# Optimization experiments

Measured on AMD Instinct MI355X. Metric: run time of the kernel, lower is better.

The kernel has to match this reference:

```python
import jax, jax.numpy as jnp
import numpy as np

B = 512      # batch
L = 20       # reviews per user/item (L1 == L2)
N = 100      # words per review (must match between user/item, required by original bmm)
V = 50000    # vocab
D = 64       # word_dim
E = 32       # id_emb_size
U = 20000    # user_num
I = 20000    # item_num
H = 3        # point_num_heads
NT, NM = 10, 12  # travel type / month cardinalities


def _lin(x, W, b):
    # torch nn.Linear: x @ W.T + b, W is [out, in]
    return x @ W.T + b


def _hard_gumbel(logits, g):
    # F.gumbel_softmax(hard=True, tau=1, dim=1); g is pre-sampled standard Gumbel noise
    y = jax.nn.softmax(logits + g, axis=1)
    hard = jax.nn.one_hot(jnp.argmax(y, axis=1), logits.shape[1], dtype=y.dtype)
    return hard - jax.lax.stop_gradient(y) + y  # straight-through


def _coatt(u_fea, i_fea, M, Wu, bu, Wi, bi, pooling, gumbel_noise=None):
    # u_fea: [B, L1, d]; i_fea: [B, L2, d]
    u = _lin(u_fea, Wu, bu)
    i = _lin(i_fea, Wi, bi)
    S = jnp.einsum('bld,de,bme->blm', u, M, i)  # [B, L1, L2]
    if pooling == 'max':
        u_score, i_score = S.max(axis=2), S.max(axis=1)
    else:
        u_score, i_score = S.mean(axis=2), S.mean(axis=1)
    if gumbel_noise is not None:
        gu, gi = gumbel_noise
        p_u, p_i = _hard_gumbel(u_score, gu), _hard_gumbel(i_score, gi)
    else:
        p_u, p_i = jax.nn.softmax(u_score, axis=1), jax.nn.softmax(i_score, axis=1)
    return p_u[..., None], p_i[..., None]  # [B, L1, 1], [B, L2, 1]


def setup_inputs() -> dict:
    key = jax.random.key(0)
    ks = iter(jax.random.split(key, 48))
    unif = lambda shape, s=0.1: jax.random.uniform(next(ks), shape, minval=-s, maxval=s, dtype=jnp.float32)
    xav = lambda shape: jax.random.normal(next(ks), shape, dtype=jnp.float32) * np.sqrt(2.0 / (shape[-1] + shape[-2]))
    inp = {}
    inp['user_reviews'] = jax.random.randint(next(ks), (B, L, N), 0, V)
    inp['item_reviews'] = jax.random.randint(next(ks), (B, L, N), 0, V)
    inp['uids'] = jax.random.randint(next(ks), (B,), 0, U)
    inp['iids'] = jax.random.randint(next(ks), (B,), 0, I)
    inp['travel_type'] = jax.random.randint(next(ks), (B,), 0, NT)
    inp['travel_month'] = jax.random.randint(next(ks), (B,), 0, NM)
    # pre-sampled standard Gumbel noise for the hard pointer selection (one per head)
    inp['gnoise_u'] = -jnp.log(-jnp.log(jax.random.uniform(next(ks), (H, B, L), minval=1e-20, maxval=1.0)))
    inp['gnoise_i'] = -jnp.log(-jnp.log(jax.random.uniform(next(ks), (H, B, L), minval=1e-20, maxval=1.0)))
    # embedding tables
    inp['user_word_embs'] = unif((V, D))
    inp['item_word_embs'] = unif((V, D))
    inp['user_id_table'] = unif((U, E), 1.0)
    inp['item_id_table'] = unif((I, E), 1.0)
    inp['type_table'] = unif((NT, E), 1.0)
    inp['month_table'] = unif((NM, E), 1.0)
    # review gate
    inp['fc_g1_w'] = unif((D, D)); inp['fc_g1_b'] = unif((D,))
    inp['fc_g2_w'] = unif((D, D)); inp['fc_g2_b'] = unif((D,))
    # per-head co-attention params (stacked over H)
    inp['M_r'] = xav((H, D, D)); inp['Wu_r'] = unif((H, D, D)); inp['bu_r'] = unif((H, D))
    inp['Wi_r'] = unif((H, D, D)); inp['bi_r'] = unif((H, D))
    inp['M_w'] = xav((H, D, D)); inp['Wu_w'] = unif((H, D, D)); inp['bu_w'] = unif((H, D))
    inp['Wi_w'] = unif((H, D, D)); inp['bi_w'] = unif((H, D))
    inp['M_f'] = xav((H, E, E)); inp['Wu_f'] = unif((H, E, E)); inp['bu_f'] = unif((H, E))
    inp['Wi_f'] = unif((H, E, E)); inp['bi_f'] = unif((H, E))
    # projection layers
    inp['ufc_w'] = unif((E, D)); inp['ufc_b'] = unif((E,))
    inp['ifc_w'] = unif((E, D)); inp['ifc_b'] = unif((E,))
    inp['u_fc_w'] = unif((E, E * H)); inp['u_fc_b'] = unif((E,))
    inp['i_fc_w'] = unif((E, E * H)); inp['i_fc_b'] = unif((E,))
    return inp


def reference(user_reviews, item_reviews, uids, iids, travel_type, travel_month,
              gnoise_u, gnoise_i, user_word_embs, item_word_embs,
              user_id_table, item_id_table, type_table, month_table,
              fc_g1_w, fc_g1_b, fc_g2_w, fc_g2_b,
              M_r, Wu_r, bu_r, Wi_r, bi_r,
              M_w, Wu_w, bu_w, Wi_w, bi_w,
              M_f, Wu_f, bu_f, Wi_f, bi_f,
              ufc_w, ufc_b, ifc_w, ifc_b, u_fc_w, u_fc_b, i_fc_w, i_fc_b):
    # id-type embeddings -> feature stack [B, 4, E]
    user_id_emb = user_id_table[uids]
    item_id_emb = item_id_table[iids]
    type_emb = type_table[travel_type]
    month_emb = month_table[travel_month]
    feature_embedding = jnp.stack([user_id_emb, item_id_emb, type_emb, month_emb], axis=1)

    def review_gate(reviews_idx, table):
        s = table[reviews_idx].sum(axis=2)  # [B, L, N, D] -> [B, L, D]
        return jax.nn.sigmoid(_lin(s, fc_g1_w, fc_g1_b)) * jnp.tanh(_lin(s, fc_g2_w, fc_g2_b))

    u_reviews_g = review_gate(user_reviews, user_word_embs)
    i_reviews_g = review_gate(item_reviews, item_word_embs)

    u_feas, i_feas = [], []
    for h in range(H):
        # review-level pointer co-attention (hard gumbel, max pooling)
        p_u, p_i = _coatt(u_reviews_g, i_reviews_g, M_r[h], Wu_r[h], bu_r[h], Wi_r[h], bi_r[h],
                          pooling='max', gumbel_noise=(gnoise_u[h], gnoise_i[h]))
        # soft index -> cast to int (kills gradient, like torch .long()) -> word gather
        u_idx = jnp.einsum('bln,bl->bn', user_reviews.astype(p_u.dtype), p_u[..., 0]).astype(jnp.int32)
        i_idx = jnp.einsum('bln,bl->bn', item_reviews.astype(p_i.dtype), p_i[..., 0]).astype(jnp.int32)
        u_words = user_word_embs[u_idx]  # [B, N, D]
        i_words = item_word_embs[i_idx]
        # word-level co-attention (softmax, avg pooling)
        p_u2, p_i2 = _coatt(u_words, i_words, M_w[h], Wu_w[h], bu_w[h], Wi_w[h], bi_w[h], pooling='avg')
        u_w_fea = jnp.einsum('bnd,bn->bd', u_words, p_u2[..., 0])
        i_w_fea = jnp.einsum('bnd,bn->bd', u_words, p_i2[..., 0])  # NOTE: original uses u_words here (kept)
        ure = jax.nn.relu(_lin(u_w_fea, ufc_w, ufc_b))  # dropout = identity (eval)
        ire = jax.nn.relu(_lin(i_w_fea, ifc_w, ifc_b))
        review_embedding = jnp.stack([ure, ire], axis=1)  # [B, 2, E]
        review_att, fea_att = _coatt(review_embedding, feature_embedding,
                                     M_f[h], Wu_f[h], bu_f[h], Wi_f[h], bi_f[h], pooling='avg')
        fea_att_e = feature_embedding * fea_att  # [B, 4, E]
        user_id_e, item_id_e, type_e, month_e = (fea_att_e[:, 0], fea_att_e[:, 1],
                                                 fea_att_e[:, 2], fea_att_e[:, 3])
        rae = review_embedding * review_att
        user_fea_h = rae[:, 0]
        u_feas.append(user_fea_h)
        i_feas.append(user_fea_h)  # NOTE: original assigns item_fea from the user slice (kept)
    u_out = _lin(jnp.concatenate(u_feas, axis=1), u_fc_w, u_fc_b)
    i_out = _lin(jnp.concatenate(i_feas, axis=1), i_fc_w, i_fc_b)
    user_fea = jnp.stack([user_id_e, type_e, u_out], axis=1)   # [B, 3, E]
    item_fea = jnp.stack([item_id_e, month_e, i_out], axis=1)  # [B, 3, E]
    return user_fea, item_fea
```

## Files before the change

### kernel.cpp

```cpp
#include <hip/hip_runtime.h>
#include <math.h>

#define Bn 512
#define Ln 20
#define Nn 100
#define Dn 64
#define En 32
#define Hn 3

__global__ __launch_bounds__(256) void k0a_prep(
    const float* __restrict__ M_r, const float* __restrict__ Wu_r, const float* __restrict__ bu_r,
    const float* __restrict__ Wi_r,
    const float* __restrict__ M_w, const float* __restrict__ Wu_w, const float* __restrict__ bu_w,
    const float* __restrict__ Wi_w, const float* __restrict__ bi_w,
    const float* __restrict__ Wu_f, const float* __restrict__ Wi_f,
    const float* __restrict__ ufc, const float* __restrict__ ifc,
    const float* __restrict__ ufc2, const float* __restrict__ ifc2,
    float* __restrict__ WiT_r, float* __restrict__ WMr, float* __restrict__ bMr,
    float* __restrict__ P, float* __restrict__ Q, float* __restrict__ MB, float* __restrict__ MTB,
    float* __restrict__ WuT_f, float* __restrict__ WiT_f,
    float* __restrict__ ufcT, float* __restrict__ ifcT,
    float* __restrict__ u_fcT, float* __restrict__ i_fcT)
{
    int t = blockIdx.x * blockDim.x + threadIdx.x;
    int stride = gridDim.x * blockDim.x;
    for (int k = t; k < Hn*Dn*Dn; k += stride) {
        int h = k >> 12, r = k & 4095; int c = r >> 6, e = r & 63;
        const float* Wu = Wu_r + h*4096; const float* M = M_r + h*4096;
        float a = 0.f;
        for (int d = 0; d < Dn; ++d) a += Wu[d*Dn + c] * M[d*Dn + e];
        WMr[k] = a;
    }
    for (int k = t; k < Hn*Dn*Dn; k += stride) {
        int h = k >> 12, r = k & 4095; int d = r >> 6, bb = r & 63;
        const float* M = M_w + h*4096; const float* Wi = Wi_w + h*4096;
        float a = 0.f;
        for (int e = 0; e < Dn; ++e) a += M[d*Dn + e] * Wi[e*Dn + bb];
        P[k] = a;
    }
    for (int k = t; k < Hn*Dn*Dn; k += stride) {
        int h = k >> 12, r = k & 4095; int d = r >> 6, bb = r & 63;
        const float* M = M_w + h*4096; const float* Wu = Wu_w + h*4096;
        float a = 0.f;
        for (int e = 0; e < Dn; ++e) a += M[e*Dn + d] * Wu[e*Dn + bb];
        Q[k] = a;
    }
    for (int k = t; k < Hn*Dn*Dn; k += stride) {
        int h = k >> 12, r = k & 4095; int c = r >> 6, dp = r & 63;
        WiT_r[k] = Wi_r[h*4096 + dp*Dn + c];
    }
    for (int k = t; k < Hn*Dn; k += stride) {
        int h = k >> 6, e = k & 63;
        const float* M = M_r + h*4096;
        float a = 0.f;
        for (int d = 0; d < Dn; ++d) a += bu_r[h*Dn + d] * M[d*Dn + e];
        bMr[k] = a;
        const float* Mw_ = M_w + h*4096;
        float p = 0.f, q = 0.f;
        for (int d2 = 0; d2 < Dn; ++d2) {
            p += Mw_[e*Dn + d2] * bi_w[h*Dn + d2];
            q += Mw_[d2*Dn + e] * bu_w[h*Dn + d2];
        }
        MB[k] = p; MTB[k] = q;
    }
    for (int k = t; k < Hn*En*En; k += stride) {
        int h = k / (En*En); int rem = k - h*En*En;
        int a = rem >> 5, c = rem & 31;
        int src = h*En*En + c*En + a;
        WuT_f[k] = Wu_f[src]; WiT_f[k] = Wi_f[src];
    }
    for (int k = t; k < Dn*En; k += stride) {
        int d = k >> 5, e = k & 31;
        ufcT[k] = ufc[e*Dn + d]; ifcT[k] = ifc[e*Dn + d];
    }
    for (int k = t; k < 96*En; k += stride) {
        int kk = k >> 5, e = k & 31;
        u_fcT[k] = ufc2[e*96 + kk]; i_fcT[k] = ifc2[e*96 + kk];
    }
}

__global__ __launch_bounds__(256) void k0b_prep(
    const float* __restrict__ Wu_w, const float* __restrict__ Wi_w,
    const float* __restrict__ P, const float* __restrict__ Q,
    const float* __restrict__ MB, const float* __restrict__ MTB,
    float* __restrict__ GuT, float* __restrict__ GiT,
    float* __restrict__ gu_v, float* __restrict__ gi_v)
{
    int t = blockIdx.x * blockDim.x + threadIdx.x;
    int stride = gridDim.x * blockDim.x;
    for (int k = t; k < Hn*Dn*Dn; k += stride) {
        int h = k >> 12, r = k & 4095; int bb = r >> 6, a = r & 63;
        const float* Wu = Wu_w + h*4096; const float* Pp = P + h*4096;
        float s = 0.f;
        for (int d = 0; d < Dn; ++d) s += Wu[d*Dn + a] * Pp[d*Dn + bb];
        GuT[k] = s;
    }
    for (int k = t; k < Hn*Dn*Dn; k += stride) {
        int h = k >> 12, r = k & 4095; int bb = r >> 6, a = r & 63;
        const float* Wi = Wi_w + h*4096; const float* Qp = Q + h*4096;
        float s = 0.f;
        for (int d = 0; d < Dn; ++d) s += Wi[d*Dn + a] * Qp[d*Dn + bb];
        GiT[k] = s;
    }
    for (int k = t; k < Hn*Dn; k += stride) {
        int h = k >> 6, a = k & 63;
        const float* Wu = Wu_w + h*4096; const float* Wi = Wi_w + h*4096;
        float s1 = 0.f, s2 = 0.f;
        for (int d = 0; d < Dn; ++d) {
            s1 += Wu[d*Dn + a] * MB[h*Dn + d];
            s2 += Wi[d*Dn + a] * MTB[h*Dn + d];
        }
        gu_v[k] = s1; gi_v[k] = s2;
    }
}

__global__ __launch_bounds__(256) void k1a_gsum(
    const int* __restrict__ urev, const int* __restrict__ irev,
    const float* __restrict__ utab, const float* __restrict__ itab,
    float* __restrict__ sout)
{
    int tid = threadIdx.x;
    int ln = tid & 63;
    int wv = tid >> 6;
    int gw = blockIdx.x * 4 + wv;
    int side = (gw >= Bn*Ln);
    int r = gw - (side ? Bn*Ln : 0);
    const int* rev = side ? irev : urev;
    const float* tab = side ? itab : utab;
    int i0 = rev[r*Nn + ln];
    int i1 = (ln < Nn - 64) ? rev[r*Nn + 64 + ln] : 0;
    int r0 = ln >> 4;
    int q4 = (ln & 15) << 2;
    float4 buf[25];
    #pragma unroll
    for (int j = 0; j < 25; ++j) {
        int n = r0 + 4*j;
        int idx = (n < 64) ? __shfl(i0, n) : __shfl(i1, n - 64);
        buf[j] = *(const float4*)(tab + idx*Dn + q4);
    }
    float4 a = buf[0];
    #pragma unroll
    for (int j = 1; j < 25; ++j) { a.x += buf[j].x; a.y += buf[j].y; a.z += buf[j].z; a.w += buf[j].w; }
    a.x += __shfl_xor(a.x, 16); a.y += __shfl_xor(a.y, 16); a.z += __shfl_xor(a.z, 16); a.w += __shfl_xor(a.w, 16);
    a.x += __shfl_xor(a.x, 32); a.y += __shfl_xor(a.y, 32); a.z += __shfl_xor(a.z, 32); a.w += __shfl_xor(a.w, 32);
    if (ln < 16) *(float4*)(sout + gw*Dn + q4) = a;
}

__global__ __launch_bounds__(256) void k1b_gate(
    const float* __restrict__ sin,
    const float* __restrict__ W1, const float* __restrict__ b1v,
    const float* __restrict__ W2, const float* __restrict__ b2v,
    float* __restrict__ ugo, float* __restrict__ igo)
{
    __shared__ float w1s[Dn][Dn+1];
    __shared__ float w2s[Dn][Dn+1];
    int tid = threadIdx.x;
    for (int k = tid; k < Dn*Dn; k += 256) {
        int r = k >> 6, c = k & 63;
        w1s[r][c] = W1[k]; w2s[r][c] = W2[k];
    }
    __syncthreads();
    int ln = tid & 63;
    int wv = tid >> 6;
    float b1 = b1v[ln], b2 = b2v[ln];
    int nW = gridDim.x * 4;
    for (int gw = blockIdx.x * 4 + wv; gw < 2*Bn*Ln; gw += nW) {
        float sv = sin[gw*Dn + ln];
        float t1 = b1, t2 = b2;
        #pragma unroll 8
        for (int d = 0; d < Dn; ++d) {
            float sd = __shfl(sv, d);
            t1 += sd * w1s[ln][d];
            t2 += sd * w2s[ln][d];
        }
        float g = (1.f / (1.f + expf(-t1))) * tanhf(t2);
        int side = (gw >= Bn*Ln);
        int r = gw - (side ? Bn*Ln : 0);
        (side ? igo : ugo)[r*Dn + ln] = g;
    }
}

__global__ __launch_bounds__(256) void k2_coatt(
    const int* __restrict__ urev, const int* __restrict__ irev,
    const int* __restrict__ uids, const int* __restrict__ iids,
    const int* __restrict__ ttype, const int* __restrict__ tmonth,
    const float* __restrict__ gu_all, const float* __restrict__ gi_all,
    const float* __restrict__ utab, const float* __restrict__ itab,
    const float* __restrict__ uid_tab, const float* __restrict__ iid_tab,
    const float* __restrict__ type_tab, const float* __restrict__ month_tab,
    const float* __restrict__ ug_in, const float* __restrict__ ig_in,
    const float* __restrict__ WMr, const float* __restrict__ bMr,
    const float* __restrict__ WiT_r, const float* __restrict__ bi_r,
    const float* __restrict__ GuT, const float* __restrict__ GiT,
    const float* __restrict__ gu_v, const float* __restrict__ gi_v,
    const float* __restrict__ M_f, const float* __restrict__ bu_f, const float* __restrict__ bi_f,
    const float* __restrict__ WuT_f, const float* __restrict__ WiT_f,
    const float* __restrict__ ufcT, const float* __restrict__ ufc_bv,
    const float* __restrict__ ifcT, const float* __restrict__ ifc_bv,
    float* __restrict__ feas, float* __restrict__ outp)
{
    __shared__ __align__(16) float big[13000];
    __shared__ float S[Ln][Ln];
    __shared__ int   lstar[2];
    __shared__ float vecs[4][Dn];
    __shared__ float sc[2][Nn];
    __shared__ float uif[2][Dn];
    __shared__ float re[2][En], fe[4][En];
    __shared__ float u3[2][En], i3[4][En], A3[2][En];
    __shared__ float att[6];

    float* ug_sp = big;
    float* ig_sp = big + 1280;
    float* pu_sp = big + 2560;
    float* pi_sp = big + 5120;
    float* Ab_sp = big + 7680;
    float* iv_sp = big + 8980;
    float* uw    = big;
    float* iw    = big + 6500;

    int tid = threadIdx.x;
    int bh = blockIdx.x;
    int b = bh / Hn;
    int h = bh - b*Hn;
    int ln = tid & 63;
    int wv = tid >> 6;

    if (tid < 4*En) {
        int rrow = tid >> 5, e = tid & 31;
        float v;
        if (rrow == 0) v = uid_tab[uids[b]*En + e];
        else if (rrow == 1) v = iid_tab[iids[b]*En + e];
        else if (rrow == 2) v = type_tab[ttype[b]*En + e];
        else v = month_tab[tmonth[b]*En + e];
        fe[rrow][e] = v;
    }
    {
        const float4* su = (const float4*)(ug_in + b*Ln*Dn);
        const float4* si = (const float4*)(ig_in + b*Ln*Dn);
        float4* du = (float4*)ug_sp;
        float4* di = (float4*)ig_sp;
        for (int k = tid; k < (Ln*Dn)/4; k += 256) { du[k] = su[k]; di[k] = si[k]; }
    }
    __syncthreads();

    {
        int mat = wv & 1;
        int dh  = wv >> 1;
        const float* W = (mat ? (WiT_r + h*4096) : (WMr + h*4096)) + dh*32*Dn + ln;
        const float* X = (mat ? ig_sp : ug_sp) + dh*32;
        float acc[Ln];
        #pragma unroll
        for (int l = 0; l < Ln; ++l) acc[l] = 0.f;
        for (int dd = 0; dd < 32; dd += 4) {
            float w0 = W[(dd+0)*Dn];
            float w1 = W[(dd+1)*Dn];
            float w2 = W[(dd+2)*Dn];
            float w3 = W[(dd+3)*Dn];
            #pragma unroll
            for (int l = 0; l < Ln; ++l) {
                float4 x = *(const float4*)(X + l*Dn + dd);
                acc[l] += x.x*w0 + x.y*w1 + x.z*w2 + x.w*w3;
            }
        }
        float* po = (mat ? pi_sp : pu_sp) + dh*(Ln*Dn) + ln;
        #pragma unroll
        for (int l = 0; l < Ln; ++l) po[l*Dn] = acc[l];
    }
    __syncthreads();
    for (int k = tid; k < 2*Ln*Dn; k += 256) {
        int mm = (k >= Ln*Dn);
        int r = k - (mm ? Ln*Dn : 0);
        int l = r >> 6, ee = r & 63;
        if (!mm) Ab_sp[l*65 + ee] = pu_sp[l*Dn + ee] + pu_sp[Ln*Dn + l*Dn + ee] + bMr[h*Dn + ee];
        else     iv_sp[l*65 + ee] = pi_sp[l*Dn + ee] + pi_sp[Ln*Dn + l*Dn + ee] + bi_r[h*Dn + ee];
    }
    __syncthreads();
    for (int k = tid; k < Ln*Ln; k += 256) {
        int l = k / Ln, m = k - l*Ln;
        float a = 0.f;
        for (int e = 0; e < Dn; ++e) a += Ab_sp[l*65 + e] * iv_sp[m*65 + e];
        S[l][m] = a;
    }
    __syncthreads();
    if (wv == 0) {
        float v = -3.4e38f;
        if (ln < Ln) {
            float mx = S[ln][0];
            #pragma unroll
            for (int m = 1; m < Ln; ++m) mx = fmaxf(mx, S[ln][m]);
            v = mx + gu_all[(h*Bn + b)*Ln + ln];
        }
        int idx = ln;
        #pragma unroll
        for (int off = 32; off > 0; off >>= 1) {
            float ov = __shfl_down(v, off);
            int oi = __shfl_down(idx, off);
            if (ov > v || (ov == v && oi < idx)) { v = ov; idx = oi; }
        }
        if (ln == 0) lstar[0] = idx;
    } else if (wv == 1) {
        float v = -3.4e38f;
        if (ln < Ln) {
            float mx = S[0][ln];
            #pragma unroll
            for (int l = 1; l < Ln; ++l) mx = fmaxf(mx, S[l][ln]);
            v = mx + gi_all[(h*Bn + b)*Ln + ln];
        }
        int idx = ln;
        #pragma unroll
        for (int off = 32; off > 0; off >>= 1) {
            float ov = __shfl_down(v, off);
            int oi = __shfl_down(idx, off);
            if (ov > v || (ov == v && oi < idx)) { v = ov; idx = oi; }
        }
        if (ln == 0) lstar[1] = idx;
    }
    __syncthreads();
    {
        const int* up = urev + (b*Ln + lstar[0])*Nn;
        const int* ip = irev + (b*Ln + lstar[1])*Nn;
        for (int k = tid; k < (Nn*Dn)/4; k += 256) {
            int n = k >> 4, q = (k & 15) << 2;
            float4 vu = *(const float4*)(utab + up[n]*Dn + q);
            float4 vi = *(const float4*)(itab + ip[n]*Dn + q);
            float* du = uw + n*65 + q;
            du[0] = vu.x; du[1] = vu.y; du[2] = vu.z; du[3] = vu.w;
            float* di = iw + n*65 + q;
            di[0] = vi.x; di[1] = vi.y; di[2] = vi.z; di[3] = vi.w;
        }
    }
    __syncthreads();
    if (tid < Dn) {
        float a = 0.f;
        for (int n = 0; n < Nn; ++n) a += uw[n*65 + tid];
        vecs[0][tid] = a * (1.f/Nn);
    } else if (tid < 2*Dn) {
        int d = tid - Dn;
        float a = 0.f;
        for (int n = 0; n < Nn; ++n) a += iw[n*65 + d];
        vecs[1][d] = a * (1.f/Nn);
    }
    __syncthreads();
    if (tid < Dn) {
        float a = gu_v[h*Dn + tid];
        for (int bb = 0; bb < Dn; ++bb) a += GuT[h*4096 + bb*Dn + tid] * vecs[1][bb];
        vecs[2][tid] = a;
    } else if (tid < 2*Dn) {
        int aa = tid - Dn;
        float a = gi_v[h*Dn + aa];
        for (int bb = 0; bb < Dn; ++bb) a += GiT[h*4096 + bb*Dn + aa] * vecs[0][bb];
        vecs[3][aa] = a;
    }
    __syncthreads();
    if (tid < Nn) {
        float a = 0.f;
        for (int d = 0; d < Dn; ++d) a += uw[tid*65 + d] * vecs[2][d];
        sc[0][tid] = a;
    } else if (tid >= 128 && tid < 128 + Nn) {
        int n = tid - 128;
        float a = 0.f;
        for (int d = 0; d < Dn; ++d) a += iw[n*65 + d] * vecs[3][d];
        sc[1][n] = a;
    }
    __syncthreads();
    if (wv == 0 || wv == 2) {
        float* s = sc[wv >> 1];
        float x0 = s[ln];
        float x1 = (ln < Nn - 64) ? s[64 + ln] : -3.4e38f;
        float mx = fmaxf(x0, x1);
        #pragma unroll
        for (int off = 32; off > 0; off >>= 1) mx = fmaxf(mx, __shfl_xor(mx, off));
        float e0 = expf(x0 - mx);
        float e1 = (ln < Nn - 64) ? expf(x1 - mx) : 0.f;
        float sum = e0 + e1;
        #pragma unroll
        for (int off = 32; off > 0; off >>= 1) sum += __shfl_xor(sum, off);
        float inv = 1.f / sum;
        s[ln] = e0 * inv;
        if (ln < Nn - 64) s[64 + ln] = e1 * inv;
    }
    __syncthreads();
    if (tid < Dn) {
        float a = 0.f;
        for (int n = 0; n < Nn; ++n) a += sc[0][n] * uw[n*65 + tid];
        uif[0][tid] = a;
    } else if (tid < 2*Dn) {
        int d = tid - Dn;
        float a = 0.f;
        for (int n = 0; n < Nn; ++n) a += sc[1][n] * uw[n*65 + d];
        uif[1][d] = a;
    }
    __syncthreads();
    if (tid < En) {
        float a = ufc_bv[tid];
        for (int d = 0; d < Dn; ++d) a += uif[0][d] * ufcT[d*En + tid];
        re[0][tid] = fmaxf(a, 0.f);
    } else if (tid < 2*En) {
        int e = tid - En;
        float a = ifc_bv[e];
        for (int d = 0; d < Dn; ++d) a += uif[1][d] * ifcT[d*En + e];
        re[1][e] = fmaxf(a, 0.f);
    }
    __syncthreads();
    const float* WuTf = WuT_f + h*En*En;
    const float* WiTf = WiT_f + h*En*En;
    const float* Mf   = M_f  + h*En*En;
    const float* buf_ = bu_f + h*En;
    const float* bif_ = bi_f + h*En;
    if (tid < 2*En) {
        int l = tid >> 5, e = tid & 31;
        float a = buf_[e];
        for (int j = 0; j < En; ++j) a += re[l][j] * WuTf[j*En + e];
        u3[l][e] = a;
    } else if (tid < 6*En) {
        int t2 = tid - 2*En;
        int m = t2 >> 5, e = t2 & 31;
        float a = bif_[e];
        for (int j = 0; j < En; ++j) a += fe[m][j] * WiTf[j*En + e];
        i3[m][e] = a;
    }
    __syncthreads();
    if (tid < 2*En) {
        int l = tid >> 5, e = tid & 31;
        float a = 0.f;
        for (int d = 0; d < En; ++d) a += u3[l][d] * Mf[d*En + e];
        A3[l][e] = a;
    }
    __syncthreads();
    if (tid == 0) {
        float S3[2][4];
        for (int l = 0; l < 2; ++l)
            for (int m = 0; m < 4; ++m) {
                float a = 0.f;
                for (int e = 0; e < En; ++e) a += A3[l][e] * i3[m][e];
                S3[l][m] = a;
            }
        float us0 = (S3[0][0] + S3[0][1] + S3[0][2] + S3[0][3]) * 0.25f;
        float us1 = (S3[1][0] + S3[1][1] + S3[1][2] + S3[1][3]) * 0.25f;
        float mx = fmaxf(us0, us1);
        float e0 = expf(us0 - mx), e1 = expf(us1 - mx);
        float inv = 1.f / (e0 + e1);
        att[0] = e0 * inv; att[1] = e1 * inv;
        float is_[4]; float mxi = -3.4e38f;
        for (int m = 0; m < 4; ++m) { is_[m] = (S3[0][m] + S3[1][m]) * 0.5f; mxi = fmaxf(mxi, is_[m]); }
        float ssum = 0.f, ee[4];
        for (int m = 0; m < 4; ++m) { ee[m] = expf(is_[m] - mxi); ssum += ee[m]; }
        float invi = 1.f / ssum;
        for (int m = 0; m < 4; ++m) att[2 + m] = ee[m] * invi;
    }
    __syncthreads();
    if (tid < En) {
        feas[b*96 + h*En + tid] = re[0][tid] * att[0];
    }
    if (h == 2) {
        if (tid >= 32 && tid < 64)        { int e = tid - 32;  outp[b*96 + e]              = fe[0][e] * att[2]; }
        else if (tid >= 64 && tid < 96)   { int e = tid - 64;  outp[b*96 + 32 + e]         = fe[2][e] * att[4]; }
        else if (tid >= 96 && tid < 128)  { int e = tid - 96;  outp[Bn*96 + b*96 + e]      = fe[1][e] * att[3]; }
        else if (tid >= 128 && tid < 160) { int e = tid - 128; outp[Bn*96 + b*96 + 32 + e] = fe[3][e] * att[5]; }
    }
}

__global__ __launch_bounds__(64) void k3_final(
    const float* __restrict__ feas,
    const float* __restrict__ u_fcT, const float* __restrict__ u_fc_bv,
    const float* __restrict__ i_fcT, const float* __restrict__ i_fc_bv,
    float* __restrict__ outp)
{
    __shared__ float f[96];
    int b = blockIdx.x, tid = threadIdx.x;
    for (int k = tid; k < 96; k += 64) f[k] = feas[b*96 + k];
    __syncthreads();
    if (tid < 32) {
        float a = u_fc_bv[tid];
        for (int k = 0; k < 96; ++k) a += f[k] * u_fcT[k*32 + tid];
        outp[b*96 + 64 + tid] = a;
    } else {
        int e = tid - 32;
        float a = i_fc_bv[e];
        for (int k = 0; k < 96; ++k) a += f[k] * i_fcT[k*32 + e];
        outp[Bn*96 + b*96 + 64 + e] = a;
    }
}

extern "C" void kernel_launch(void* const* d_in, const int* in_sizes, int n_in,
                              void* d_out, int out_size, void* d_ws, size_t ws_size,
                              hipStream_t stream)
{
    const int* urev = (const int*)d_in[0];
    const int* irev = (const int*)d_in[1];
    const int* uids = (const int*)d_in[2];
    const int* iids = (const int*)d_in[3];
    const int* ttype = (const int*)d_in[4];
    const int* tmonth = (const int*)d_in[5];
    const float* gu = (const float*)d_in[6];
    const float* gi = (const float*)d_in[7];
    const float* utab = (const float*)d_in[8];
    const float* itab = (const float*)d_in[9];
    const float* uid_tab = (const float*)d_in[10];
    const float* iid_tab = (const float*)d_in[11];
    const float* type_tab = (const float*)d_in[12];
    const float* month_tab = (const float*)d_in[13];
    const float* fc_g1_w = (const float*)d_in[14];
    const float* fc_g1_b = (const float*)d_in[15];
    const float* fc_g2_w = (const float*)d_in[16];
    const float* fc_g2_b = (const float*)d_in[17];
    const float* M_r = (const float*)d_in[18];
    const float* Wu_r = (const float*)d_in[19];
    const float* bu_r = (const float*)d_in[20];
    const float* Wi_r = (const float*)d_in[21];
    const float* bi_r = (const float*)d_in[22];
    const float* M_w = (const float*)d_in[23];
    const float* Wu_w = (const float*)d_in[24];
    const float* bu_w = (const float*)d_in[25];
    const float* Wi_w = (const float*)d_in[26];
    const float* bi_w = (const float*)d_in[27];
    const float* M_f = (const float*)d_in[28];
    const float* Wu_f = (const float*)d_in[29];
    const float* bu_f = (const float*)d_in[30];
    const float* Wi_f = (const float*)d_in[31];
    const float* bi_f = (const float*)d_in[32];
    const float* ufc_w = (const float*)d_in[33];
    const float* ufc_b = (const float*)d_in[34];
    const float* ifc_w = (const float*)d_in[35];
    const float* ifc_b = (const float*)d_in[36];
    const float* u_fc_w = (const float*)d_in[37];
    const float* u_fc_b = (const float*)d_in[38];
    const float* i_fc_w = (const float*)d_in[39];
    const float* i_fc_b = (const float*)d_in[40];
    (void)in_sizes; (void)n_in; (void)out_size; (void)ws_size;

    float* ws = (float*)d_ws;
    float* ugo   = ws;
    float* igo   = ugo + Bn*Ln*Dn;
    float* sgat  = igo + Bn*Ln*Dn;
    float* feas  = sgat + 2*Bn*Ln*Dn;
    float* WiT_r = feas + Bn*96;
    float* WMr   = WiT_r + Hn*Dn*Dn;
    float* bMr   = WMr + Hn*Dn*Dn;
    float* P     = bMr + Hn*Dn;
    float* Q     = P + Hn*Dn*Dn;
    float* MB    = Q + Hn*Dn*Dn;
    float* MTB   = MB + Hn*Dn;
    float* GuT   = MTB + Hn*Dn;
    float* GiT   = GuT + Hn*Dn*Dn;
    float* gu_v  = GiT + Hn*Dn*Dn;
    float* gi_v  = gu_v + Hn*Dn;
    float* WuT_f = gi_v + Hn*Dn;
    float* WiT_f = WuT_f + Hn*En*En;
    float* ufcT  = WiT_f + Hn*En*En;
    float* ifcT  = ufcT + Dn*En;
    float* u_fcT = ifcT + Dn*En;
    float* i_fcT = u_fcT + 96*En;

    hipLaunchKernelGGL(k0a_prep, dim3(48), dim3(256), 0, stream,
        M_r, Wu_r, bu_r, Wi_r, M_w, Wu_w, bu_w, Wi_w, bi_w,
        Wu_f, Wi_f, ufc_w, ifc_w, u_fc_w, i_fc_w,
        WiT_r, WMr, bMr, P, Q, MB, MTB, WuT_f, WiT_f, ufcT, ifcT, u_fcT, i_fcT);

    hipLaunchKernelGGL(k0b_prep, dim3(48), dim3(256), 0, stream,
        Wu_w, Wi_w, P, Q, MB, MTB, GuT, GiT, gu_v, gi_v);

    hipLaunchKernelGGL(k1a_gsum, dim3(2*Bn*Ln/4), dim3(256), 0, stream,
        urev, irev, utab, itab, sgat);

    hipLaunchKernelGGL(k1b_gate, dim3(512), dim3(256), 0, stream,
        sgat, fc_g1_w, fc_g1_b, fc_g2_w, fc_g2_b, ugo, igo);

    hipLaunchKernelGGL(k2_coatt, dim3(Bn*Hn), dim3(256), 0, stream,
        urev, irev, uids, iids, ttype, tmonth, gu, gi, utab, itab,
        uid_tab, iid_tab, type_tab, month_tab, ugo, igo,
        WMr, bMr, WiT_r, bi_r, GuT, GiT, gu_v, gi_v,
        M_f, bu_f, bi_f, WuT_f, WiT_f,
        ufcT, ufc_b, ifcT, ifc_b, feas, (float*)d_out);

    hipLaunchKernelGGL(k3_final, dim3(Bn), dim3(64), 0, stream,
        feas, u_fcT, u_fc_b, i_fcT, i_fc_b, (float*)d_out);
}
```

Before: 326.5 us.

## Shrink coattention kernel shared memory and restructure word gathers for occupancy

Shrinks k2_coatt's shared memory from a roughly 52KB region to a 25KB pool. It does this by swapping padded arrays for XOR-swizzled layouts and splitting the review projection across waves by row rather than by reduction half, which removes the partial-sum reduction pass. Only the user review's words are staged in shared memory. The item review's words are gathered straight from global memory into registers and reduced with wave shuffles, and the second gather is repeated for the score step. The aim is to fit more blocks per CU (launch bounds set to 4) and drop a sync and reduction stage, at the cost of repeating global gathers for the item table.

Result: no change. 326.7 us (+0.1%).

```diff
diff --git a/kernel.cpp b/kernel.cpp
--- a/kernel.cpp
+++ b/kernel.cpp
@@ -180,7 +180,7 @@
     }
 }
 
-__global__ __launch_bounds__(256) void k2_coatt(
+__global__ __launch_bounds__(256, 4) void k2_coatt(
     const int* __restrict__ urev, const int* __restrict__ irev,
     const int* __restrict__ uids, const int* __restrict__ iids,
     const int* __restrict__ ttype, const int* __restrict__ tmonth,
@@ -199,24 +199,12 @@
     const float* __restrict__ ifcT, const float* __restrict__ ifc_bv,
     float* __restrict__ feas, float* __restrict__ outp)
 {
-    __shared__ __align__(16) float big[13000];
-    __shared__ float S[Ln][Ln];
-    __shared__ int   lstar[2];
+    __shared__ __align__(16) float pool[6400];
     __shared__ float vecs[4][Dn];
     __shared__ float sc[2][Nn];
     __shared__ float uif[2][Dn];
-    __shared__ float re[2][En], fe[4][En];
-    __shared__ float u3[2][En], i3[4][En], A3[2][En];
     __shared__ float att[6];
-
-    float* ug_sp = big;
-    float* ig_sp = big + 1280;
-    float* pu_sp = big + 2560;
-    float* pi_sp = big + 5120;
-    float* Ab_sp = big + 7680;
-    float* iv_sp = big + 8980;
-    float* uw    = big;
-    float* iw    = big + 6500;
+    __shared__ int   lstar[2];
 
     int tid = threadIdx.x;
     int bh = blockIdx.x;
@@ -225,69 +213,58 @@
     int ln = tid & 63;
     int wv = tid >> 6;
 
-    if (tid < 4*En) {
-        int rrow = tid >> 5, e = tid & 31;
-        float v;
-        if (rrow == 0) v = uid_tab[uids[b]*En + e];
-        else if (rrow == 1) v = iid_tab[iids[b]*En + e];
-        else if (rrow == 2) v = type_tab[ttype[b]*En + e];
-        else v = month_tab[tmonth[b]*En + e];
-        fe[rrow][e] = v;
-    }
     {
         const float4* su = (const float4*)(ug_in + b*Ln*Dn);
         const float4* si = (const float4*)(ig_in + b*Ln*Dn);
-        float4* du = (float4*)ug_sp;
-        float4* di = (float4*)ig_sp;
+        float4* du = (float4*)pool;
+        float4* di = (float4*)(pool + 1280);
         for (int k = tid; k < (Ln*Dn)/4; k += 256) { du[k] = su[k]; di[k] = si[k]; }
     }
     __syncthreads();
 
     {
-        int mat = wv & 1;
-        int dh  = wv >> 1;
-        const float* W = (mat ? (WiT_r + h*4096) : (WMr + h*4096)) + dh*32*Dn + ln;
-        const float* X = (mat ? ig_sp : ug_sp) + dh*32;
-        float acc[Ln];
-        #pragma unroll
-        for (int l = 0; l < Ln; ++l) acc[l] = 0.f;
-        for (int dd = 0; dd < 32; dd += 4) {
+        int iside = wv >> 1;
+        int lbase = (wv & 1) * 10;
+        const float* W = (iside ? (WiT_r + h*4096) : (WMr + h*4096)) + ln;
+        const float* X = pool + (iside ? 1280 : 0);
+        float bias = iside ? bi_r[h*Dn + ln] : bMr[h*Dn + ln];
+        float acc[10];
+        #pragma unroll
+        for (int l = 0; l < 10; ++l) acc[l] = 0.f;
+        for (int dd = 0; dd < Dn; dd += 4) {
             float w0 = W[(dd+0)*Dn];
             float w1 = W[(dd+1)*Dn];
             float w2 = W[(dd+2)*Dn];
             float w3 = W[(dd+3)*Dn];
             #pragma unroll
-            for (int l = 0; l < Ln; ++l) {
-                float4 x = *(const float4*)(X + l*Dn + dd);
+            for (int l = 0; l < 10; ++l) {
+                float4 x = *(const float4*)(X + (lbase+l)*Dn + dd);
                 acc[l] += x.x*w0 + x.y*w1 + x.z*w2 + x.w*w3;
             }
         }
-        float* po = (mat ? pi_sp : pu_sp) + dh*(Ln*Dn) + ln;
-        #pragma unroll
-        for (int l = 0; l < Ln; ++l) po[l*Dn] = acc[l];
-    }
-    __syncthreads();
-    for (int k = tid; k < 2*Ln*Dn; k += 256) {
-        int mm = (k >= Ln*Dn);
-        int r = k - (mm ? Ln*Dn : 0);
-        int l = r >> 6, ee = r & 63;
-        if (!mm) Ab_sp[l*65 + ee] = pu_sp[l*Dn + ee] + pu_sp[Ln*Dn + l*Dn + ee] + bMr[h*Dn + ee];
-        else     iv_sp[l*65 + ee] = pi_sp[l*Dn + ee] + pi_sp[Ln*Dn + l*Dn + ee] + bi_r[h*Dn + ee];
+        float* out = pool + (iside ? 3840 : 2560);
+        #pragma unroll
+        for (int l = 0; l < 10; ++l) {
+            int lg = lbase + l;
+            out[lg*Dn + (ln ^ lg)] = acc[l] + bias;
+        }
     }
     __syncthreads();
     for (int k = tid; k < Ln*Ln; k += 256) {
         int l = k / Ln, m = k - l*Ln;
-        float a = 0.f;
-        for (int e = 0; e < Dn; ++e) a += Ab_sp[l*65 + e] * iv_sp[m*65 + e];
-        S[l][m] = a;
+        const float* Ab = pool + 2560 + l*Dn;
+        const float* iv = pool + 3840 + m*Dn;
+        float a = 0.f;
+        for (int e = 0; e < Dn; ++e) a += Ab[e ^ l] * iv[e ^ m];
+        pool[5120 + k] = a;
     }
     __syncthreads();
     if (wv == 0) {
         float v = -3.4e38f;
         if (ln < Ln) {
-            float mx = S[ln][0];
+            float mx = pool[5120 + ln*Ln];
             #pragma unroll
-            for (int m = 1; m < Ln; ++m) mx = fmaxf(mx, S[ln][m]);
+            for (int m = 1; m < Ln; ++m) mx = fmaxf(mx, pool[5120 + ln*Ln + m]);
             v = mx + gu_all[(h*Bn + b)*Ln + ln];
         }
         int idx = ln;
@@ -301,9 +278,9 @@
     } else if (wv == 1) {
         float v = -3.4e38f;
         if (ln < Ln) {
-            float mx = S[0][ln];
+            float mx = pool[5120 + ln];
             #pragma unroll
-            for (int l = 1; l < Ln; ++l) mx = fmaxf(mx, S[l][ln]);
+            for (int l = 1; l < Ln; ++l) mx = fmaxf(mx, pool[5120 + l*Ln + ln]);
             v = mx + gi_all[(h*Bn + b)*Ln + ln];
         }
         int idx = ln;
@@ -316,31 +293,48 @@
         if (ln == 0) lstar[1] = idx;
     }
     __syncthreads();
-    {
-        const int* up = urev + (b*Ln + lstar[0])*Nn;
-        const int* ip = irev + (b*Ln + lstar[1])*Nn;
-        for (int k = tid; k < (Nn*Dn)/4; k += 256) {
-            int n = k >> 4, q = (k & 15) << 2;
-            float4 vu = *(const float4*)(utab + up[n]*Dn + q);
-            float4 vi = *(const float4*)(itab + ip[n]*Dn + q);
-            float* du = uw + n*65 + q;
-            du[0] = vu.x; du[1] = vu.y; du[2] = vu.z; du[3] = vu.w;
-            float* di = iw + n*65 + q;
-            di[0] = vi.x; di[1] = vi.y; di[2] = vi.z; di[3] = vi.w;
-        }
-    }
-    __syncthreads();
-    if (tid < Dn) {
-        float a = 0.f;
-        for (int n = 0; n < Nn; ++n) a += uw[n*65 + tid];
-        vecs[0][tid] = a * (1.f/Nn);
-    } else if (tid < 2*Dn) {
-        int d = tid - Dn;
-        float a = 0.f;
-        for (int n = 0; n < Nn; ++n) a += iw[n*65 + d];
-        vecs[1][d] = a * (1.f/Nn);
-    }
-    __syncthreads();
+
+    int rubase = (b*Ln + lstar[0])*Nn;
+    int ribase = (b*Ln + lstar[1])*Nn;
+    int r0 = ln >> 4;
+    int q4 = (ln & 15) << 2;
+    int idxr[25];
+
+    if (wv < 2) {
+        for (int k = tid; k < Nn*16; k += 128) {
+            int n = k >> 4, qi = k & 15;
+            int idx = urev[rubase + n];
+            float4 v = *(const float4*)(utab + idx*Dn + (qi << 2));
+            *(float4*)(pool + n*Dn + (((qi ^ (n & 15)) << 2))) = v;
+        }
+    } else {
+        const int* rev = (wv == 2) ? irev : urev;
+        const float* tab = (wv == 2) ? itab : utab;
+        int rb = (wv == 2) ? ribase : rubase;
+        #pragma unroll
+        for (int j = 0; j < 25; ++j) idxr[j] = rev[rb + r0 + 4*j];
+        float4 s = make_float4(0.f, 0.f, 0.f, 0.f);
+        #pragma unroll 5
+        for (int g = 0; g < 5; ++g) {
+            float4 v0 = *(const float4*)(tab + idxr[g*5+0]*Dn + q4);
+            float4 v1 = *(const float4*)(tab + idxr[g*5+1]*Dn + q4);
+            float4 v2 = *(const float4*)(tab + idxr[g*5+2]*Dn + q4);
+            float4 v3 = *(const float4*)(tab + idxr[g*5+3]*Dn + q4);
+            float4 v4 = *(const float4*)(tab + idxr[g*5+4]*Dn + q4);
+            s.x += v0.x+v1.x+v2.x+v3.x+v4.x;
+            s.y += v0.y+v1.y+v2.y+v3.y+v4.y;
+            s.z += v0.z+v1.z+v2.z+v3.z+v4.z;
+            s.w += v0.w+v1.w+v2.w+v3.w+v4.w;
+        }
+        s.x += __shfl_xor(s.x, 16); s.y += __shfl_xor(s.y, 16); s.z += __shfl_xor(s.z, 16); s.w += __shfl_xor(s.w, 16);
+        s.x += __shfl_xor(s.x, 32); s.y += __shfl_xor(s.y, 32); s.z += __shfl_xor(s.z, 32); s.w += __shfl_xor(s.w, 32);
+        if (ln < 16) {
+            float4 m = make_float4(s.x*(1.f/Nn), s.y*(1.f/Nn), s.z*(1.f/Nn), s.w*(1.f/Nn));
+            *(float4*)(&vecs[(wv == 2) ? 1 : 0][q4]) = m;
+        }
+    }
+    __syncthreads();
+
     if (tid < Dn) {
         float a = gu_v[h*Dn + tid];
         for (int bb = 0; bb < Dn; ++bb) a += GuT[h*4096 + bb*Dn + tid] * vecs[1][bb];
@@ -352,15 +346,49 @@
         vecs[3][aa] = a;
     }
     __syncthreads();
+
     if (tid < Nn) {
         float a = 0.f;
-        for (int d = 0; d < Dn; ++d) a += uw[tid*65 + d] * vecs[2][d];
+        const float* row = pool + tid*Dn;
+        int sw = tid & 15;
+        #pragma unroll
+        for (int qi = 0; qi < 16; ++qi) {
+            float4 w = *(const float4*)(&vecs[2][qi << 2]);
+            float4 x = *(const float4*)(row + ((qi ^ sw) << 2));
+            a += x.x*w.x + x.y*w.y + x.z*w.z + x.w*w.w;
+        }
         sc[0][tid] = a;
-    } else if (tid >= 128 && tid < 128 + Nn) {
-        int n = tid - 128;
-        float a = 0.f;
-        for (int d = 0; d < Dn; ++d) a += iw[n*65 + d] * vecs[3][d];
-        sc[1][n] = a;
+    } else if (wv == 2) {
+        float4 wq = *(const float4*)(&vecs[3][q4]);
+        #pragma unroll 5
+        for (int g = 0; g < 5; ++g) {
+            float p0, p1, p2, p3, p4;
+            {
+                float4 v0 = *(const float4*)(itab + idxr[g*5+0]*Dn + q4);
+                float4 v1 = *(const float4*)(itab + idxr[g*5+1]*Dn + q4);
+                float4 v2 = *(const float4*)(itab + idxr[g*5+2]*Dn + q4);
+                float4 v3 = *(const float4*)(itab + idxr[g*5+3]*Dn + q4);
+                float4 v4 = *(const float4*)(itab + idxr[g*5+4]*Dn + q4);
+                p0 = v0.x*wq.x + v0.y*wq.y + v0.z*wq.z + v0.w*wq.w;
+                p1 = v1.x*wq.x + v1.y*wq.y + v1.z*wq.z + v1.w*wq.w;
+                p2 = v2.x*wq.x + v2.y*wq.y + v2.z*wq.z + v2.w*wq.w;
+                p3 = v3.x*wq.x + v3.y*wq.y + v3.z*wq.z + v3.w*wq.w;
+                p4 = v4.x*wq.x + v4.y*wq.y + v4.z*wq.z + v4.w*wq.w;
+            }
+            #pragma unroll
+            for (int off = 1; off < 16; off <<= 1) {
+                p0 += __shfl_xor(p0, off); p1 += __shfl_xor(p1, off);
+                p2 += __shfl_xor(p2, off); p3 += __shfl_xor(p3, off);
+                p4 += __shfl_xor(p4, off);
+            }
+            if ((ln & 15) == 0) {
+                sc[1][r0 + 4*(g*5+0)] = p0;
+                sc[1][r0 + 4*(g*5+1)] = p1;
+                sc[1][r0 + 4*(g*5+2)] = p2;
+                sc[1][r0 + 4*(g*5+3)] = p3;
+                sc[1][r0 + 4*(g*5+4)] = p4;
+            }
+        }
     }
     __syncthreads();
     if (wv == 0 || wv == 2) {
@@ -380,51 +408,63 @@
         if (ln < Nn - 64) s[64 + ln] = e1 * inv;
     }
     __syncthreads();
-    if (tid < Dn) {
-        float a = 0.f;
-        for (int n = 0; n < Nn; ++n) a += sc[0][n] * uw[n*65 + tid];
-        uif[0][tid] = a;
-    } else if (tid < 2*Dn) {
-        int d = tid - Dn;
-        float a = 0.f;
-        for (int n = 0; n < Nn; ++n) a += sc[1][n] * uw[n*65 + d];
-        uif[1][d] = a;
-    }
-    __syncthreads();
+    if (tid < 2*Dn) {
+        int which = tid >> 6;
+        int d = tid & 63;
+        int qt = (d >> 2), dl = d & 3;
+        const float* p = sc[which];
+        float a = 0.f;
+        for (int n = 0; n < Nn; ++n)
+            a += p[n] * pool[n*Dn + ((qt ^ (n & 15)) << 2) + dl];
+        uif[which][d] = a;
+    }
+    __syncthreads();
+    float* fe_ = pool;
+    float* re_ = pool + 128;
+    float* u3_ = pool + 192;
+    float* i3_ = pool + 256;
+    float* A3_ = pool + 384;
     if (tid < En) {
         float a = ufc_bv[tid];
         for (int d = 0; d < Dn; ++d) a += uif[0][d] * ufcT[d*En + tid];
-        re[0][tid] = fmaxf(a, 0.f);
+        re_[tid] = fmaxf(a, 0.f);
     } else if (tid < 2*En) {
         int e = tid - En;
         float a = ifc_bv[e];
         for (int d = 0; d < Dn; ++d) a += uif[1][d] * ifcT[d*En + e];
-        re[1][e] = fmaxf(a, 0.f);
+        re_[En + e] = fmaxf(a, 0.f);
+    } else if (tid < 2*En + 4*En) {
+        int j = tid - 2*En;
+        int rrow = j >> 5, e = j & 31;
+        float v;
+        if (rrow == 0) v = uid_tab[uids[b]*En + e];
+        else if (rrow == 1) v = iid_tab[iids[b]*En + e];
+        else if (rrow == 2) v = type_tab[ttype[b]*En + e];
+        else v = month_tab[tmonth[b]*En + e];
+        fe_[j] = v;
     }
     __syncthreads();
     const float* WuTf = WuT_f + h*En*En;
     const float* WiTf = WiT_f + h*En*En;
     const float* Mf   = M_f  + h*En*En;
-    const float* buf_ = bu_f + h*En;
-    const float* bif_ = bi_f + h*En;
     if (tid < 2*En) {
         int l = tid >> 5, e = tid & 31;
-        float a = buf_[e];
-        for (int j = 0; j < En; ++j) a += re[l][j] * WuTf[j*En + e];
-        u3[l][e] = a;
+        float a = bu_f[h*En + e];
+        for (int j = 0; j < En; ++j) a += re_[l*En + j] * WuTf[j*En + e];
+        u3_[tid] = a;
     } else if (tid < 6*En) {
         int t2 = tid - 2*En;
         int m = t2 >> 5, e = t2 & 31;
-        float a = bif_[e];
-        for (int j = 0; j < En; ++j) a += fe[m][j] * WiTf[j*En + e];
-        i3[m][e] = a;
+        float a = bi_f[h*En + e];
+        for (int j = 0; j < En; ++j) a += fe_[m*En + j] * WiTf[j*En + e];
+        i3_[t2] = a;
     }
     __syncthreads();
     if (tid < 2*En) {
         int l = tid >> 5, e = tid & 31;
         float a = 0.f;
-        for (int d = 0; d < En; ++d) a += u3[l][d] * Mf[d*En + e];
-        A3[l][e] = a;
+        for (int d = 0; d < En; ++d) a += u3_[l*En + d] * Mf[d*En + e];
+        A3_[tid] = a;
     }
     __syncthreads();
     if (tid == 0) {
@@ -432,7 +472,7 @@
         for (int l = 0; l < 2; ++l)
             for (int m = 0; m < 4; ++m) {
                 float a = 0.f;
-                for (int e = 0; e < En; ++e) a += A3[l][e] * i3[m][e];
+                for (int e = 0; e < En; ++e) a += A3_[l*En + e] * i3_[m*En + e];
                 S3[l][m] = a;
             }
         float us0 = (S3[0][0] + S3[0][1] + S3[0][2] + S3[0][3]) * 0.25f;
@@ -450,13 +490,13 @@
     }
     __syncthreads();
     if (tid < En) {
-        feas[b*96 + h*En + tid] = re[0][tid] * att[0];
+        feas[b*96 + h*En + tid] = re_[tid] * att[0];
     }
     if (h == 2) {
-        if (tid >= 32 && tid < 64)        { int e = tid - 32;  outp[b*96 + e]              = fe[0][e] * att[2]; }
-        else if (tid >= 64 && tid < 96)   { int e = tid - 64;  outp[b*96 + 32 + e]         = fe[2][e] * att[4]; }
-        else if (tid >= 96 && tid < 128)  { int e = tid - 96;  outp[Bn*96 + b*96 + e]      = fe[1][e] * att[3]; }
-        else if (tid >= 128 && tid < 160) { int e = tid - 128; outp[Bn*96 + b*96 + 32 + e] = fe[3][e] * att[5]; }
+        if (tid >= 32 && tid < 64)        { int e = tid - 32;  outp[b*96 + e]              = fe_[e]      * att[2]; }
+        else if (tid >= 64 && tid < 96)   { int e = tid - 64;  outp[b*96 + 32 + e]         = fe_[64 + e] * att[4]; }
+        else if (tid >= 96 && tid < 128)  { int e = tid - 96;  outp[Bn*96 + b*96 + e]      = fe_[32 + e] * att[3]; }
+        else if (tid >= 128 && tid < 160) { int e = tid - 128; outp[Bn*96 + b*96 + 32 + e] = fe_[96 + e] * att[5]; }
     }
 }
 
```
